# Kernel optimization log

Measured on AMD Instinct MI355X. Metric: run time of the kernel, lower is better.

Reference implementation:

```python
import jax, jax.numpy as jnp
import numpy as np

B, S, HID = 1, 2048, 2048
H, HKV, D = 32, 8, 64
G = H // HKV  # query heads per kv head


def rotate_half(x):
    x1, x2 = jnp.split(x, 2, axis=-1)
    return jnp.concatenate([-x2, x1], axis=-1)


def setup_inputs() -> dict:
    key = jax.random.key(0)
    ks = jax.random.split(key, 7)
    hidden_states = jax.random.normal(ks[0], (B, S, HID), dtype=jnp.float32)
    # RoPE tables (any broadcastable values work for correctness; use real angles)
    inv_freq = 1.0 / (10000.0 ** (np.arange(0, D, 2, dtype=np.float32) / D))
    ang = np.arange(S, dtype=np.float32)[:, None] * inv_freq[None, :]  # [S, D/2]
    ang = np.concatenate([ang, ang], axis=-1)  # [S, D]
    cos = jnp.asarray(np.cos(ang))[None, None]  # [1,1,S,D]
    sin = jnp.asarray(np.sin(ang))[None, None]
    sc = 0.02
    Wq = jax.random.normal(ks[1], (H * D, HID), dtype=jnp.float32) * sc
    Wk = jax.random.normal(ks[2], (HKV * D, HID), dtype=jnp.float32) * sc
    Wv = jax.random.normal(ks[3], (HKV * D, HID), dtype=jnp.float32) * sc
    Wo = jax.random.normal(ks[4], (HID, H * D), dtype=jnp.float32) * sc
    return {"hidden_states": hidden_states, "cos": cos, "sin": sin,
            "Wq": Wq, "Wk": Wk, "Wv": Wv, "Wo": Wo}


def reference(hidden_states, cos, sin, Wq, Wk, Wv, Wo):
    b, s, _ = hidden_states.shape
    # projections (torch Linear: x @ W^T)
    q = jnp.einsum('bsh,oh->bso', hidden_states, Wq).reshape(b, s, H, D).transpose(0, 2, 1, 3)   # [B,H,S,D]
    k = jnp.einsum('bsh,oh->bso', hidden_states, Wk).reshape(b, s, HKV, D).transpose(0, 2, 1, 3)  # [B,Hkv,S,D]
    v = jnp.einsum('bsh,oh->bso', hidden_states, Wv).reshape(b, s, HKV, D).transpose(0, 2, 1, 3)
    # RoPE
    q = q * cos + rotate_half(q) * sin
    k = k * cos + rotate_half(k) * sin
    # GQA: group query heads instead of repeat_interleave-ing KV
    qg = q.reshape(b, HKV, G, s, D)
    scores = jnp.einsum('bkgsd,bktd->bkgst', qg, k) / jnp.sqrt(jnp.asarray(D, q.dtype))
    causal = jnp.tril(jnp.ones((s, s), dtype=bool))
    scores = jnp.where(causal, scores, jnp.asarray(-jnp.inf, scores.dtype))
    probs = jax.nn.softmax(scores.astype(jnp.float32), axis=-1).astype(q.dtype)
    ctx = jnp.einsum('bkgst,bktd->bkgsd', probs, v)  # [B,Hkv,G,S,D]
    ctx = ctx.reshape(b, H, s, D).transpose(0, 2, 1, 3).reshape(b, s, H * D)
    return jnp.einsum('bso,ho->bsh', ctx, Wo)
```

## Files before the change

### kernel.cpp

```cpp
#include <hip/hip_runtime.h>

typedef unsigned short u16;
typedef __bf16 bf16x8 __attribute__((ext_vector_type(8)));
typedef float f32x4 __attribute__((ext_vector_type(4)));
typedef float f32x16 __attribute__((ext_vector_type(16)));

static __device__ __forceinline__ u16 f2bf(float f) {
  unsigned u = __builtin_bit_cast(unsigned, f);
  u += 0x7fffu + ((u >> 16) & 1u);
  return (u16)(u >> 16);
}
static __device__ __forceinline__ float bf2f(u16 u) {
  return __builtin_bit_cast(float, (unsigned)u << 16);
}
static __device__ __forceinline__ unsigned cvtpk(float lo, float hi) {
  unsigned r;
  asm("v_cvt_pk_bf16_f32 %0, %1, %2" : "=v"(r) : "v"(lo), "v"(hi));
  return r;
}
static __device__ __forceinline__ float fexp2(float x) {
  float r;
  asm("v_exp_f32 %0, %1" : "=v"(r) : "v"(x));
  return r;
}

static __device__ __forceinline__ void gload_lds16(const void* g, void* l) {
  __builtin_amdgcn_global_load_lds((const __attribute__((address_space(1))) unsigned int*)g,
                                   (__attribute__((address_space(3))) unsigned int*)l,
                                   16, 0, 0);
}

__global__ __launch_bounds__(256) void cvt_all(
    const float* __restrict__ X, const float* __restrict__ Wq, const float* __restrict__ Wk,
    const float* __restrict__ Wv, const float* __restrict__ Wo,
    u16* __restrict__ oX, u16* __restrict__ oWq, u16* __restrict__ oWk,
    u16* __restrict__ oWv, u16* __restrict__ oWo) {
  const int b = blockIdx.x;
  const float* s; u16* d; int lb;
  if (b < 1024)      { s = X;  d = oX;  lb = b; }
  else if (b < 2048) { s = Wq; d = oWq; lb = b - 1024; }
  else if (b < 2304) { s = Wk; d = oWk; lb = b - 2048; }
  else if (b < 2560) { s = Wv; d = oWv; lb = b - 2304; }
  else               { s = Wo; d = oWo; lb = b - 2560; }
  const int base = lb * 4096 + threadIdx.x * 4;
#pragma unroll
  for (int j = 0; j < 4; ++j) {
    const int off = base + j * 1024;
    float4 v = *(const float4*)(s + off);
    ushort4 u;
    u.x = f2bf(v.x); u.y = f2bf(v.y); u.z = f2bf(v.z); u.w = f2bf(v.w);
    *(ushort4*)(d + off) = u;
  }
}

__global__ __launch_bounds__(256, 4) void gemm_qkv(
    const u16* __restrict__ A, const u16* __restrict__ Bq, const u16* __restrict__ Bk,
    const u16* __restrict__ Bv, u16* __restrict__ Qb, u16* __restrict__ Kb,
    u16* __restrict__ Vt, const float* __restrict__ cosp, const float* __restrict__ sinp) {
  __shared__ u16 As[64 * 64];
  __shared__ u16 Bs[128 * 64];
  const int tid = threadIdx.x;
  const int lane = tid & 63, w = tid >> 6;
  const int wr = w >> 1, wc = w & 1;
  const int lr = lane & 15, lq = lane >> 4;
  const int bm = blockIdx.y << 6;
  const int bn = blockIdx.x << 7;
  const int K = 2048;

  const u16* Bp; int nb, region;
  if (bn < 2048)      { Bp = Bq; nb = bn;        region = 0; }
  else if (bn < 2560) { Bp = Bk; nb = bn - 2048; region = 1; }
  else                { Bp = Bv; nb = bn - 2560; region = 2; }

  f32x4 acc[2][4] = {};

  for (int kt = 0; kt < 32; ++kt) {
    const int k0 = kt << 6;
#pragma unroll
    for (int i = 0; i < 2; ++i) {
      const int cid = (i << 8) + tid;
      const int r = cid >> 3, c = cid & 7;
      const int cs = (c ^ (r & 7)) << 3;
      gload_lds16(A + (size_t)(bm + r) * K + k0 + cs, (char*)As + cid * 16);
    }
#pragma unroll
    for (int i = 0; i < 4; ++i) {
      const int cid = (i << 8) + tid;
      const int r = cid >> 3, c = cid & 7;
      const int cs = (c ^ (r & 7)) << 3;
      gload_lds16(Bp + (size_t)(nb + r) * K + k0 + cs, (char*)Bs + cid * 16);
    }
    __syncthreads();
    bf16x8 af[2][2], bfv[2][4];
#pragma unroll
    for (int ks = 0; ks < 2; ++ks) {
#pragma unroll
      for (int f = 0; f < 2; ++f) {
        const int ra = wr * 32 + f * 16 + lr;
        const int ca = (lq + (ks << 2)) ^ (ra & 7);
        af[ks][f] = *(const bf16x8*)&As[((ra << 3) | ca) << 3];
      }
#pragma unroll
      for (int f = 0; f < 4; ++f) {
        const int rb = wc * 64 + f * 16 + lr;
        const int cb = (lq + (ks << 2)) ^ (rb & 7);
        bfv[ks][f] = *(const bf16x8*)&Bs[((rb << 3) | cb) << 3];
      }
    }
#pragma unroll
    for (int ks = 0; ks < 2; ++ks)
#pragma unroll
      for (int mf = 0; mf < 2; ++mf)
#pragma unroll
        for (int nf = 0; nf < 4; ++nf)
          acc[mf][nf] = __builtin_amdgcn_mfma_f32_16x16x32_bf16(
              af[ks][mf], bfv[ks][nf], acc[mf][nf], 0, 0, 0);
    __syncthreads();
  }

  const int rbase = bm + wr * 32;
  const int cb64 = nb + wc * 64;
  if (region == 2) {
    const int hkv = cb64 >> 6;
#pragma unroll
    for (int mf = 0; mf < 2; ++mf) {
      const int s0 = rbase + mf * 16 + lq * 4;
#pragma unroll
      for (int nf = 0; nf < 4; ++nf) {
        const int d = (cb64 & 63) + nf * 16 + lr;
        ushort4 st;
        st.x = f2bf(acc[mf][nf][0]); st.y = f2bf(acc[mf][nf][1]);
        st.z = f2bf(acc[mf][nf][2]); st.w = f2bf(acc[mf][nf][3]);
        *(ushort4*)&Vt[(size_t)hkv * 131072 + (size_t)d * 2048 + s0] = st;
      }
    }
  } else {
    u16* outp = region ? Kb : Qb;
    const int ldo = region ? 512 : 2048;
    const float post = region ? 1.0f : 0.18033688011112042f;
#pragma unroll
    for (int mf = 0; mf < 2; ++mf)
#pragma unroll
      for (int r = 0; r < 4; ++r) {
        const int s = rbase + mf * 16 + lq * 4 + r;
        const float* cr = cosp + s * 64;
        const float* sr = sinp + s * 64;
#pragma unroll
        for (int nf = 0; nf < 2; ++nf) {
          const int d1 = nf * 16 + lr, d2 = d1 + 32;
          const float x1 = acc[mf][nf][r], x2 = acc[mf][nf + 2][r];
          const float y1 = (x1 * cr[d1] - x2 * sr[d1]) * post;
          const float y2 = (x2 * cr[d2] + x1 * sr[d2]) * post;
          outp[(size_t)s * ldo + cb64 + d1] = f2bf(y1);
          outp[(size_t)s * ldo + cb64 + d2] = f2bf(y2);
        }
      }
  }
}

__global__ __launch_bounds__(256, 4) void gemm_out(
    const u16* __restrict__ A, const u16* __restrict__ B, float* __restrict__ C,
    int M, int N, int K) {
  __shared__ u16 As[64 * 64];
  __shared__ u16 Bs[128 * 64];
  const int tid = threadIdx.x;
  const int lane = tid & 63, w = tid >> 6;
  const int wr = w >> 1, wc = w & 1;
  const int lr = lane & 15, lq = lane >> 4;
  const int bm = blockIdx.y << 6, bn = blockIdx.x << 7;

  f32x4 acc[2][4] = {};
  const int nK = K >> 6;
  for (int kt = 0; kt < nK; ++kt) {
    const int k0 = kt << 6;
#pragma unroll
    for (int i = 0; i < 2; ++i) {
      const int cid = (i << 8) + tid;
      const int r = cid >> 3, c = cid & 7;
      const int cs = (c ^ (r & 7)) << 3;
      gload_lds16(A + (size_t)(bm + r) * K + k0 + cs, (char*)As + cid * 16);
    }
#pragma unroll
    for (int i = 0; i < 4; ++i) {
      const int cid = (i << 8) + tid;
      const int r = cid >> 3, c = cid & 7;
      const int cs = (c ^ (r & 7)) << 3;
      gload_lds16(B + (size_t)(bn + r) * K + k0 + cs, (char*)Bs + cid * 16);
    }
    __syncthreads();
    bf16x8 af[2][2], bfv[2][4];
#pragma unroll
    for (int ks = 0; ks < 2; ++ks) {
#pragma unroll
      for (int f = 0; f < 2; ++f) {
        const int ra = wr * 32 + f * 16 + lr;
        const int ca = (lq + (ks << 2)) ^ (ra & 7);
        af[ks][f] = *(const bf16x8*)&As[((ra << 3) | ca) << 3];
      }
#pragma unroll
      for (int f = 0; f < 4; ++f) {
        const int rb = wc * 64 + f * 16 + lr;
        const int cb = (lq + (ks << 2)) ^ (rb & 7);
        bfv[ks][f] = *(const bf16x8*)&Bs[((rb << 3) | cb) << 3];
      }
    }
#pragma unroll
    for (int ks = 0; ks < 2; ++ks)
#pragma unroll
      for (int mf = 0; mf < 2; ++mf)
#pragma unroll
        for (int nf = 0; nf < 4; ++nf)
          acc[mf][nf] = __builtin_amdgcn_mfma_f32_16x16x32_bf16(
              af[ks][mf], bfv[ks][nf], acc[mf][nf], 0, 0, 0);
    __syncthreads();
  }
  const int rbase = bm + wr * 32;
  const int cbase = bn + wc * 64;
#pragma unroll
  for (int mf = 0; mf < 2; ++mf)
#pragma unroll
    for (int r = 0; r < 4; ++r) {
      const int s = rbase + mf * 16 + lq * 4 + r;
#pragma unroll
      for (int nf = 0; nf < 4; ++nf)
        C[(size_t)s * N + cbase + nf * 16 + lr] = acc[mf][nf][r];
    }
}

__global__ __launch_bounds__(512, 4) void attn_v12(
    const u16* __restrict__ Qb, const u16* __restrict__ Kb,
    const u16* __restrict__ Vt, u16* __restrict__ P0, u16* __restrict__ P1,
    u16* __restrict__ P2, float* __restrict__ lsum) {
  __shared__ u16 Ks[2][4096];
  __shared__ u16 Vs[2][4096];
  const int hkv = blockIdx.x / 3;
  const int ck = blockIdx.x % 3;
  const int by = blockIdx.y;
  const int j = (by & 1) ? (by >> 1) : (31 - (by >> 1));
  const int tid = threadIdx.x;
  const int w = tid >> 6, lane = tid & 63;
  const int col = lane & 31, hi = lane >> 5;
  const int g = col >> 3, r = col & 7;
  const int h = hkv * 4 + g;

  const int qoff = w * 8 + r;
  const int qg = j * 64 + qoff;

  u16* Pc = (ck == 0) ? P0 : (ck == 1) ? P1 : P2;

  const u16* qp = Qb + (size_t)qg * 2048 + h * 64 + hi * 8;
  uint4 qf[4];
#pragma unroll
  for (int s = 0; s < 4; ++s) qf[s] = *(const uint4*)(qp + 16 * s);

  f32x16 o0 = {}, o1 = {};
  float l_loc = 0.f;

  auto STAGE = [&](int buf, int t) {
    const int kv0 = t << 6;
    const int rr = tid >> 3, cc = tid & 7;
    const int csw = (cc ^ (rr & 7)) << 3;
    gload_lds16(Kb + (size_t)(kv0 + rr) * 512 + hkv * 64 + csw,
                (char*)Ks + buf * 8192 + tid * 16);
    gload_lds16(Vt + (size_t)hkv * 131072 + (size_t)rr * 2048 + kv0 + csw,
                (char*)Vs + buf * 8192 + tid * 16);
  };

  if (ck <= j) {
    STAGE(0, ck);
    int i = 0;
    for (int t = ck; t <= j; t += 3, ++i) {
      const int buf = i & 1;
      __syncthreads();
      if (t + 3 <= j) STAGE(buf ^ 1, t + 3);
      const char* Kl = (const char*)Ks + buf * 8192;
      const char* Vl = (const char*)Vs + buf * 8192;

      f32x16 sc0 = {}, sc1 = {};
#pragma unroll
      for (int s = 0; s < 4; ++s) {
        const int c = 2 * s + hi;
        const bf16x8 k0 = *(const bf16x8*)(Kl + (((col) << 3) + (c ^ (col & 7))) * 16);
        sc0 = __builtin_amdgcn_mfma_f32_32x32x16_bf16(
            k0, __builtin_bit_cast(bf16x8, qf[s]), sc0, 0, 0, 0);
        const bf16x8 k1 = *(const bf16x8*)(Kl + (((col + 32) << 3) + (c ^ (col & 7))) * 16);
        sc1 = __builtin_amdgcn_mfma_f32_32x32x16_bf16(
            k1, __builtin_bit_cast(bf16x8, qf[s]), sc1, 0, 0, 0);
      }

      if (t == j) {
#pragma unroll
        for (int i2 = 0; i2 < 16; ++i2) {
          const int kvr = (i2 & 3) + 8 * (i2 >> 2) + 4 * hi;
          if (kvr > qoff) sc0[i2] = -1e30f;
          if (kvr + 32 > qoff) sc1[i2] = -1e30f;
        }
      }

      float p0[16], p1[16];
#pragma unroll
      for (int i2 = 0; i2 < 16; ++i2) { p0[i2] = fexp2(sc0[i2]); p1[i2] = fexp2(sc1[i2]); }

      float r0 = 0.f, r1 = 0.f, r2 = 0.f, r3 = 0.f;
#pragma unroll
      for (int i2 = 0; i2 < 4; ++i2) {
        r0 += p0[4 * i2]     + p1[4 * i2];
        r1 += p0[4 * i2 + 1] + p1[4 * i2 + 1];
        r2 += p0[4 * i2 + 2] + p1[4 * i2 + 2];
        r3 += p0[4 * i2 + 3] + p1[4 * i2 + 3];
      }
      l_loc += (r0 + r1) + (r2 + r3);

      unsigned W0a[4], W1a[4], W0b[4], W1b[4];
#pragma unroll
      for (int gg = 0; gg < 4; ++gg) {
        W0a[gg] = cvtpk(p0[4 * gg], p0[4 * gg + 1]);
        W1a[gg] = cvtpk(p0[4 * gg + 2], p0[4 * gg + 3]);
        W0b[gg] = cvtpk(p1[4 * gg], p1[4 * gg + 1]);
        W1b[gg] = cvtpk(p1[4 * gg + 2], p1[4 * gg + 3]);
      }

#pragma unroll
      for (int s2 = 0; s2 < 4; ++s2) {
        const unsigned* W0 = (s2 & 2) ? W0b : W0a;
        const unsigned* W1 = (s2 & 2) ? W1b : W1a;
        const int G = s2 & 1, ga = 2 * G, gb = 2 * G + 1;
        const unsigned sx0 = hi ? W0[ga] : W0[gb];
        const unsigned sx1 = hi ? W1[ga] : W1[gb];
        const unsigned rx0 = __shfl_xor(sx0, 32, 64);
        const unsigned rx1 = __shfl_xor(sx1, 32, 64);
        uint4 pw;
        pw.x = hi ? rx0 : W0[ga];
        pw.y = hi ? rx1 : W1[ga];
        pw.z = hi ? W0[gb] : rx0;
        pw.w = hi ? W1[gb] : rx1;
        const bf16x8 pf = __builtin_bit_cast(bf16x8, pw);
        const int c = 2 * s2 + hi;
        const bf16x8 v0 = *(const bf16x8*)(Vl + (((col) << 3) + (c ^ (col & 7))) * 16);
        const bf16x8 v1 = *(const bf16x8*)(Vl + (((col + 32) << 3) + (c ^ (col & 7))) * 16);
        o0 = __builtin_amdgcn_mfma_f32_32x32x16_bf16(v0, pf, o0, 0, 0, 0);
        o1 = __builtin_amdgcn_mfma_f32_32x32x16_bf16(v1, pf, o1, 0, 0, 0);
      }
    }
  }

  const float l = l_loc + __shfl_xor(l_loc, 32, 64);

  u16* op = Pc + (size_t)qg * 2048 + h * 64;
#pragma unroll
  for (int gg = 0; gg < 4; ++gg) {
    uint2 s0, s1;
    s0.x = cvtpk(o0[4 * gg], o0[4 * gg + 1]);
    s0.y = cvtpk(o0[4 * gg + 2], o0[4 * gg + 3]);
    s1.x = cvtpk(o1[4 * gg], o1[4 * gg + 1]);
    s1.y = cvtpk(o1[4 * gg + 2], o1[4 * gg + 3]);
    *(uint2*)(op + 8 * gg + 4 * hi)      = s0;
    *(uint2*)(op + 8 * gg + 4 * hi + 32) = s1;
  }
  if (hi == 0)
    lsum[(size_t)ck * 65536 + (size_t)qg * 32 + h] = l;
}

__global__ __launch_bounds__(256) void attn_merge3(
    u16* __restrict__ P0, const u16* __restrict__ P1, const u16* __restrict__ P2,
    const float* __restrict__ lsum) {
  const int s = blockIdx.x;
  const int e0 = threadIdx.x * 8;
  const int h = e0 >> 6;
  const float l = lsum[(size_t)s * 32 + h] + lsum[65536 + (size_t)s * 32 + h] +
                  lsum[131072 + (size_t)s * 32 + h];
  const float inv = 1.f / l;
  uint4 a = *(const uint4*)(P0 + (size_t)s * 2048 + e0);
  uint4 b = *(const uint4*)(P1 + (size_t)s * 2048 + e0);
  uint4 d = *(const uint4*)(P2 + (size_t)s * 2048 + e0);
  const u16* pa = (const u16*)&a;
  const u16* pb = (const u16*)&b;
  const u16* pd = (const u16*)&d;
  ushort4 oA, oB;
  oA.x = f2bf((bf2f(pa[0]) + bf2f(pb[0]) + bf2f(pd[0])) * inv);
  oA.y = f2bf((bf2f(pa[1]) + bf2f(pb[1]) + bf2f(pd[1])) * inv);
  oA.z = f2bf((bf2f(pa[2]) + bf2f(pb[2]) + bf2f(pd[2])) * inv);
  oA.w = f2bf((bf2f(pa[3]) + bf2f(pb[3]) + bf2f(pd[3])) * inv);
  oB.x = f2bf((bf2f(pa[4]) + bf2f(pb[4]) + bf2f(pd[4])) * inv);
  oB.y = f2bf((bf2f(pa[5]) + bf2f(pb[5]) + bf2f(pd[5])) * inv);
  oB.z = f2bf((bf2f(pa[6]) + bf2f(pb[6]) + bf2f(pd[6])) * inv);
  oB.w = f2bf((bf2f(pa[7]) + bf2f(pb[7]) + bf2f(pd[7])) * inv);
  *(ushort4*)(P0 + (size_t)s * 2048 + e0)     = oA;
  *(ushort4*)(P0 + (size_t)s * 2048 + e0 + 4) = oB;
}

extern "C" void kernel_launch(void* const* d_in, const int* in_sizes, int n_in,
                              void* d_out, int out_size, void* d_ws, size_t ws_size,
                              hipStream_t stream) {
  const float* X    = (const float*)d_in[0];
  const float* cosp = (const float*)d_in[1];
  const float* sinp = (const float*)d_in[2];
  const float* Wq   = (const float*)d_in[3];
  const float* Wk   = (const float*)d_in[4];
  const float* Wv   = (const float*)d_in[5];
  const float* Wo   = (const float*)d_in[6];

  u16* ws  = (u16*)d_ws;
  u16* Xb  = ws;
  u16* Wqb = ws + 4194304;
  u16* Wkb = ws + 8388608;
  u16* Wvb = ws + 9437184;
  u16* Wob = ws + 10485760;
  u16* Qb  = ws + 14680064;
  u16* Kb  = ws + 18874368;
  u16* Vt  = ws + 19922944;
  u16* P2  = ws + 20971520;
  u16* P0  = Xb;
  u16* P1  = Wqb;
  float* lsum = (float*)(ws + 8388608);

  cvt_all<<<3584, 256, 0, stream>>>(X, Wq, Wk, Wv, Wo, Xb, Wqb, Wkb, Wvb, Wob);

  dim3 gqkv(24, 32), ga(24, 32), go(16, 32);
  gemm_qkv<<<gqkv, 256, 0, stream>>>(Xb, Wqb, Wkb, Wvb, Qb, Kb, Vt, cosp, sinp);
  attn_v12<<<ga, 512, 0, stream>>>(Qb, Kb, Vt, P0, P1, P2, lsum);
  attn_merge3<<<2048, 256, 0, stream>>>(P0, P1, P2, lsum);
  gemm_out<<<go, 256, 0, stream>>>(P0, Wob, (float*)d_out, 2048, 2048, 2048);
}
```

Measured before the change: 122.2 us.

## Process two KV tiles per barrier with quad-buffered shared memory in attention

```diff
diff --git a/kernel.cpp b/kernel.cpp
--- a/kernel.cpp
+++ b/kernel.cpp
@@ -227,12 +227,12 @@
     }
 }
 
-__global__ __launch_bounds__(512, 4) void attn_v12(
+__global__ __launch_bounds__(512, 4) void attn_v14(
     const u16* __restrict__ Qb, const u16* __restrict__ Kb,
     const u16* __restrict__ Vt, u16* __restrict__ P0, u16* __restrict__ P1,
     u16* __restrict__ P2, float* __restrict__ lsum) {
-  __shared__ u16 Ks[2][4096];
-  __shared__ u16 Vs[2][4096];
+  __shared__ u16 Ks[4][4096];
+  __shared__ u16 Vs[4][4096];
   const int hkv = blockIdx.x / 3;
   const int ck = blockIdx.x % 3;
   const int by = blockIdx.y;
@@ -256,91 +256,95 @@
   f32x16 o0 = {}, o1 = {};
   float l_loc = 0.f;
 
-  auto STAGE = [&](int buf, int t) {
+  auto STAGE1 = [&](int slot, int t) {
     const int kv0 = t << 6;
     const int rr = tid >> 3, cc = tid & 7;
     const int csw = (cc ^ (rr & 7)) << 3;
     gload_lds16(Kb + (size_t)(kv0 + rr) * 512 + hkv * 64 + csw,
-                (char*)Ks + buf * 8192 + tid * 16);
+                (char*)Ks + slot * 8192 + tid * 16);
     gload_lds16(Vt + (size_t)hkv * 131072 + (size_t)rr * 2048 + kv0 + csw,
-                (char*)Vs + buf * 8192 + tid * 16);
+                (char*)Vs + slot * 8192 + tid * 16);
   };
+  auto STAGE2 = [&](int pb, int t) {
+    STAGE1(pb * 2, t);
+    if (t + 3 <= j) STAGE1(pb * 2 + 1, t + 3);
+  };
+
+  auto TILE = [&](const char* Kl, const char* Vl, bool diag) {
+    f32x16 sc0 = {}, sc1 = {};
+#pragma unroll
+    for (int s = 0; s < 4; ++s) {
+      const int c = 2 * s + hi;
+      const bf16x8 k0 = *(const bf16x8*)(Kl + (((col) << 3) + (c ^ (col & 7))) * 16);
+      sc0 = __builtin_amdgcn_mfma_f32_32x32x16_bf16(
+          k0, __builtin_bit_cast(bf16x8, qf[s]), sc0, 0, 0, 0);
+      const bf16x8 k1 = *(const bf16x8*)(Kl + (((col + 32) << 3) + (c ^ (col & 7))) * 16);
+      sc1 = __builtin_amdgcn_mfma_f32_32x32x16_bf16(
+          k1, __builtin_bit_cast(bf16x8, qf[s]), sc1, 0, 0, 0);
+    }
+    if (diag) {
+#pragma unroll
+      for (int i2 = 0; i2 < 16; ++i2) {
+        const int kvr = (i2 & 3) + 8 * (i2 >> 2) + 4 * hi;
+        if (kvr > qoff) sc0[i2] = -1e30f;
+        if (kvr + 32 > qoff) sc1[i2] = -1e30f;
+      }
+    }
+    float p0[16], p1[16];
+#pragma unroll
+    for (int i2 = 0; i2 < 16; ++i2) { p0[i2] = fexp2(sc0[i2]); p1[i2] = fexp2(sc1[i2]); }
+    float r0 = 0.f, r1 = 0.f, r2 = 0.f, r3 = 0.f;
+#pragma unroll
+    for (int i2 = 0; i2 < 4; ++i2) {
+      r0 += p0[4 * i2]     + p1[4 * i2];
+      r1 += p0[4 * i2 + 1] + p1[4 * i2 + 1];
+      r2 += p0[4 * i2 + 2] + p1[4 * i2 + 2];
+      r3 += p0[4 * i2 + 3] + p1[4 * i2 + 3];
+    }
+    l_loc += (r0 + r1) + (r2 + r3);
+    unsigned W0a[4], W1a[4], W0b[4], W1b[4];
+#pragma unroll
+    for (int gg = 0; gg < 4; ++gg) {
+      W0a[gg] = cvtpk(p0[4 * gg], p0[4 * gg + 1]);
+      W1a[gg] = cvtpk(p0[4 * gg + 2], p0[4 * gg + 3]);
+      W0b[gg] = cvtpk(p1[4 * gg], p1[4 * gg + 1]);
+      W1b[gg] = cvtpk(p1[4 * gg + 2], p1[4 * gg + 3]);
+    }
+#pragma unroll
+    for (int s2 = 0; s2 < 4; ++s2) {
+      const unsigned* W0 = (s2 & 2) ? W0b : W0a;
+      const unsigned* W1 = (s2 & 2) ? W1b : W1a;
+      const int G = s2 & 1, ga = 2 * G, gb = 2 * G + 1;
+      const unsigned sx0 = hi ? W0[ga] : W0[gb];
+      const unsigned sx1 = hi ? W1[ga] : W1[gb];
+      const unsigned rx0 = __shfl_xor(sx0, 32, 64);
+      const unsigned rx1 = __shfl_xor(sx1, 32, 64);
+      uint4 pw;
+      pw.x = hi ? rx0 : W0[ga];
+      pw.y = hi ? rx1 : W1[ga];
+      pw.z = hi ? W0[gb] : rx0;
+      pw.w = hi ? W1[gb] : rx1;
+      const bf16x8 pf = __builtin_bit_cast(bf16x8, pw);
+      const int c = 2 * s2 + hi;
+      const bf16x8 v0 = *(const bf16x8*)(Vl + (((col) << 3) + (c ^ (col & 7))) * 16);
+      const bf16x8 v1 = *(const bf16x8*)(Vl + (((col + 32) << 3) + (c ^ (col & 7))) * 16);
+      o0 = __builtin_amdgcn_mfma_f32_32x32x16_bf16(v0, pf, o0, 0, 0, 0);
+      o1 = __builtin_amdgcn_mfma_f32_32x32x16_bf16(v1, pf, o1, 0, 0, 0);
+    }
+  };
 
   if (ck <= j) {
-    STAGE(0, ck);
-    int i = 0;
-    for (int t = ck; t <= j; t += 3, ++i) {
-      const int buf = i & 1;
+    STAGE2(0, ck);
+    int ipair = 0;
+    for (int t = ck; t <= j; t += 6, ++ipair) {
+      const int pb = ipair & 1;
       __syncthreads();
-      if (t + 3 <= j) STAGE(buf ^ 1, t + 3);
-      const char* Kl = (const char*)Ks + buf * 8192;
-      const char* Vl = (const char*)Vs + buf * 8192;
-
-      f32x16 sc0 = {}, sc1 = {};
-#pragma unroll
-      for (int s = 0; s < 4; ++s) {
-        const int c = 2 * s + hi;
-        const bf16x8 k0 = *(const bf16x8*)(Kl + (((col) << 3) + (c ^ (col & 7))) * 16);
-        sc0 = __builtin_amdgcn_mfma_f32_32x32x16_bf16(
-            k0, __builtin_bit_cast(bf16x8, qf[s]), sc0, 0, 0, 0);
-        const bf16x8 k1 = *(const bf16x8*)(Kl + (((col + 32) << 3) + (c ^ (col & 7))) * 16);
-        sc1 = __builtin_amdgcn_mfma_f32_32x32x16_bf16(
-            k1, __builtin_bit_cast(bf16x8, qf[s]), sc1, 0, 0, 0);
-      }
-
-      if (t == j) {
-#pragma unroll
-        for (int i2 = 0; i2 < 16; ++i2) {
-          const int kvr = (i2 & 3) + 8 * (i2 >> 2) + 4 * hi;
-          if (kvr > qoff) sc0[i2] = -1e30f;
-          if (kvr + 32 > qoff) sc1[i2] = -1e30f;
-        }
-      }
-
-      float p0[16], p1[16];
-#pragma unroll
-      for (int i2 = 0; i2 < 16; ++i2) { p0[i2] = fexp2(sc0[i2]); p1[i2] = fexp2(sc1[i2]); }
-
-      float r0 = 0.f, r1 = 0.f, r2 = 0.f, r3 = 0.f;
-#pragma unroll
-      for (int i2 = 0; i2 < 4; ++i2) {
-        r0 += p0[4 * i2]     + p1[4 * i2];
-        r1 += p0[4 * i2 + 1] + p1[4 * i2 + 1];
-        r2 += p0[4 * i2 + 2] + p1[4 * i2 + 2];
-        r3 += p0[4 * i2 + 3] + p1[4 * i2 + 3];
-      }
-      l_loc += (r0 + r1) + (r2 + r3);
-
-      unsigned W0a[4], W1a[4], W0b[4], W1b[4];
-#pragma unroll
-      for (int gg = 0; gg < 4; ++gg) {
-        W0a[gg] = cvtpk(p0[4 * gg], p0[4 * gg + 1]);
-        W1a[gg] = cvtpk(p0[4 * gg + 2], p0[4 * gg + 3]);
-        W0b[gg] = cvtpk(p1[4 * gg], p1[4 * gg + 1]);
-        W1b[gg] = cvtpk(p1[4 * gg + 2], p1[4 * gg + 3]);
-      }
-
-#pragma unroll
-      for (int s2 = 0; s2 < 4; ++s2) {
-        const unsigned* W0 = (s2 & 2) ? W0b : W0a;
-        const unsigned* W1 = (s2 & 2) ? W1b : W1a;
-        const int G = s2 & 1, ga = 2 * G, gb = 2 * G + 1;
-        const unsigned sx0 = hi ? W0[ga] : W0[gb];
-        const unsigned sx1 = hi ? W1[ga] : W1[gb];
-        const unsigned rx0 = __shfl_xor(sx0, 32, 64);
-        const unsigned rx1 = __shfl_xor(sx1, 32, 64);
-        uint4 pw;
-        pw.x = hi ? rx0 : W0[ga];
-        pw.y = hi ? rx1 : W1[ga];
-        pw.z = hi ? W0[gb] : rx0;
-        pw.w = hi ? W1[gb] : rx1;
-        const bf16x8 pf = __builtin_bit_cast(bf16x8, pw);
-        const int c = 2 * s2 + hi;
-        const bf16x8 v0 = *(const bf16x8*)(Vl + (((col) << 3) + (c ^ (col & 7))) * 16);
-        const bf16x8 v1 = *(const bf16x8*)(Vl + (((col + 32) << 3) + (c ^ (col & 7))) * 16);
-        o0 = __builtin_amdgcn_mfma_f32_32x32x16_bf16(v0, pf, o0, 0, 0, 0);
-        o1 = __builtin_amdgcn_mfma_f32_32x32x16_bf16(v1, pf, o1, 0, 0, 0);
-      }
+      if (t + 6 <= j) STAGE2(pb ^ 1, t + 6);
+      TILE((const char*)Ks + (pb * 2) * 8192,
+           (const char*)Vs + (pb * 2) * 8192, t == j);
+      if (t + 3 <= j)
+        TILE((const char*)Ks + (pb * 2 + 1) * 8192,
+             (const char*)Vs + (pb * 2 + 1) * 8192, t + 3 == j);
     }
   }
 
@@ -418,7 +422,7 @@
 
   dim3 gqkv(24, 32), ga(24, 32), go(16, 32);
   gemm_qkv<<<gqkv, 256, 0, stream>>>(Xb, Wqb, Wkb, Wvb, Qb, Kb, Vt, cosp, sinp);
-  attn_v12<<<ga, 512, 0, stream>>>(Qb, Kb, Vt, P0, P1, P2, lsum);
+  attn_v14<<<ga, 512, 0, stream>>>(Qb, Kb, Vt, P0, P1, P2, lsum);
   attn_merge3<<<2048, 256, 0, stream>>>(P0, P1, P2, lsum);
   gemm_out<<<go, 256, 0, stream>>>(P0, Wob, (float*)d_out, 2048, 2048, 2048);
 }
```

New measurement: 122.1 us, median of 2. Within noise of the previous version (-0.0%).
